# Performance work log

Measured on AMD Instinct MI355X. Metric: run time of the kernel, lower is better.

The kernel has to match this reference:

```python
import jax, jax.numpy as jnp
import numpy as np

EMBED_DIM = 768
Q_DIM = 64
V_DIM = 64
WINDOW_SIZE = 3


def setup_inputs() -> dict:
    key = jax.random.key(0)
    ks = jax.random.split(key, 7)
    B, N = 4, 4096
    s = 1.0 / np.sqrt(EMBED_DIM)
    x = jax.random.normal(ks[0], (B, N, EMBED_DIM), dtype=jnp.float32)
    Wq = jax.random.normal(ks[1], (EMBED_DIM, Q_DIM), dtype=jnp.float32) * s
    bq = jax.random.normal(ks[2], (Q_DIM,), dtype=jnp.float32) * 0.01
    Wk = jax.random.normal(ks[3], (EMBED_DIM, Q_DIM), dtype=jnp.float32) * s
    bk = jax.random.normal(ks[4], (Q_DIM,), dtype=jnp.float32) * 0.01
    Wv = jax.random.normal(ks[5], (EMBED_DIM, V_DIM), dtype=jnp.float32) * s
    bv = jax.random.normal(ks[6], (V_DIM,), dtype=jnp.float32) * 0.01
    return {"x": x, "Wq": Wq, "bq": bq, "Wk": Wk, "bk": bk, "Wv": Wv, "bv": bv}


def reference(x, Wq, bq, Wk, bk, Wv, bv):
    # Faithful translation of SliddingWindowAttention.forward, including the
    # original's quirk: diagonal scores are written into columns 0..window_size-1
    # of a full (B, N, N) zero matrix, softmax is taken over ALL N columns
    # (zeros included), and the result is matmul'd with V.
    B, N, _ = x.shape
    Q = x @ Wq + bq  # (B, N, Q_DIM)
    K = x @ Wk + bk  # (B, N, Q_DIM)
    V = x @ Wv + bv  # (B, N, V_DIM)

    half = WINDOW_SIZE // 2
    columns = jnp.zeros((B, N, N), dtype=x.dtype)
    for idx, di in enumerate(range(-half, half + 1)):
        # diagonal offset di: pair row i with column j = i + di (valid rows only)
        rows = np.arange(max(0, -di), N - max(0, di))
        cols_j = rows + di
        c = jnp.einsum('bid,bid->bi', Q[:, rows, :], K[:, cols_j, :])
        columns = columns.at[:, rows, idx].set(c)

    attn = jax.nn.softmax(columns, axis=2)  # (B, N, N)
    return attn @ V  # (B, N, V_DIM)
```

## Files before the change

### kernel.cpp

```cpp
#include <hip/hip_runtime.h>
#include <hip/hip_bf16.h>
#include <math.h>

#define EMBED 768
#define NTOK  4096
#define NB    4
#define ROWS  16384
#define CN    192

typedef __attribute__((ext_vector_type(8))) short bf16x8;
typedef __attribute__((ext_vector_type(8))) unsigned short u16x8;
typedef __attribute__((ext_vector_type(4))) float f32x4;

__device__ inline void split2(float f, short& h, short& l) {
  union { float f; unsigned u; } a; a.f = f;
  unsigned r = (a.u + 0x7FFFu + ((a.u >> 16) & 1u)) & 0xFFFF0000u;
  h = (short)(r >> 16);
  union { unsigned u; float f; } hf; hf.u = r;
  union { float f; unsigned u; } b; b.f = f - hf.f;
  l = (short)((b.u + 0x7FFFu + ((b.u >> 16) & 1u)) >> 16);
}

__global__ __launch_bounds__(256) void wprep(const float* __restrict__ Wq,
                                             const float* __restrict__ Wk,
                                             const float* __restrict__ Wv,
                                             unsigned short* __restrict__ Wt,
                                             float* __restrict__ Vsum) {
  __shared__ float tile[32 * 64];
  const int b   = blockIdx.x;
  const int mat = b / 24;
  const int ks  = b - mat * 24;
  const float* W = (mat == 0) ? Wq : (mat == 1) ? Wk : Wv;
  const int t = threadIdx.x;

  const float4* src = (const float4*)(W + ks * 2048);
  ((float4*)tile)[t]       = src[t];
  ((float4*)tile)[t + 256] = src[t + 256];
  __syncthreads();

  const int q    = t >> 6;
  const int nloc = t & 63;
  u16x8 hv, lv;
#pragma unroll
  for (int j = 0; j < 8; ++j) {
    short h, l;
    split2(tile[(q * 8 + j) * 64 + nloc], h, l);
    hv[j] = (unsigned short)h;
    lv[j] = (unsigned short)l;
  }
  const size_t base = (size_t)ks * 12288 + (size_t)q * 1536 + (size_t)(mat * 64 + nloc) * 8;
  *(u16x8*)(Wt + base)        = hv;
  *(u16x8*)(Wt + base + 6144) = lv;

  if (b == 0 && t < NB * 64) Vsum[t] = 0.f;
}


__device__ inline void splitHW(float f, short& h, short& l) {
  __hip_bfloat16 hb = __float2bfloat16(f);
  float hf = __bfloat162float(hb);
  __hip_bfloat16 lb = __float2bfloat16(f - hf);
  h = __builtin_bit_cast(short, hb);
  l = __builtin_bit_cast(short, lb);
}

__device__ inline void cvt8hw(const float4 f0, const float4 f1, bf16x8& h, bf16x8& l) {
  short hh, ll;
  splitHW(f0.x, hh, ll); h[0] = hh; l[0] = ll;
  splitHW(f0.y, hh, ll); h[1] = hh; l[1] = ll;
  splitHW(f0.z, hh, ll); h[2] = hh; l[2] = ll;
  splitHW(f0.w, hh, ll); h[3] = hh; l[3] = ll;
  splitHW(f1.x, hh, ll); h[4] = hh; l[4] = ll;
  splitHW(f1.y, hh, ll); h[5] = hh; l[5] = ll;
  splitHW(f1.z, hh, ll); h[6] = hh; l[6] = ll;
  splitHW(f1.w, hh, ll); h[7] = hh; l[7] = ll;
}

#define LOADB(H0, L0, H1, L1, H2, L2, KS) do {                        \
    const bf16x8* _p = (const bf16x8*)(Bb + (size_t)(KS) * 12288);    \
    H0 = _p[0];  L0 = _p[768];                                        \
    H1 = _p[16]; L1 = _p[784];                                        \
    H2 = _p[32]; L2 = _p[800];                                        \
  } while (0)

#define LOADA(A0, A1, KS) do {                                        \
    A0 = *(const float4*)(xa + (KS) * 32);                            \
    A1 = *(const float4*)(xa + (KS) * 32 + 4);                        \
  } while (0)

#define COMPUTE(A0, A1, H0, L0, H1, L1, H2, L2) do {                              \
    bf16x8 ah, al;                                                                \
    cvt8hw(A0, A1, ah, al);                                                       \
    acc0 = __builtin_amdgcn_mfma_f32_16x16x32_bf16(ah, H0, acc0, 0, 0, 0);        \
    acc1 = __builtin_amdgcn_mfma_f32_16x16x32_bf16(ah, H1, acc1, 0, 0, 0);        \
    acc2 = __builtin_amdgcn_mfma_f32_16x16x32_bf16(ah, H2, acc2, 0, 0, 0);        \
    acc0 = __builtin_amdgcn_mfma_f32_16x16x32_bf16(ah, L0, acc0, 0, 0, 0);        \
    acc1 = __builtin_amdgcn_mfma_f32_16x16x32_bf16(ah, L1, acc1, 0, 0, 0);        \
    acc2 = __builtin_amdgcn_mfma_f32_16x16x32_bf16(ah, L2, acc2, 0, 0, 0);        \
    acc0 = __builtin_amdgcn_mfma_f32_16x16x32_bf16(al, H0, acc0, 0, 0, 0);        \
    acc1 = __builtin_amdgcn_mfma_f32_16x16x32_bf16(al, H1, acc1, 0, 0, 0);        \
    acc2 = __builtin_amdgcn_mfma_f32_16x16x32_bf16(al, H2, acc2, 0, 0, 0);        \
  } while (0)

__global__ __launch_bounds__(512, 4) void qkv_mfma(const float* __restrict__ x,
                                                   const unsigned short* __restrict__ Wtu,
                                                   const float* __restrict__ bq,
                                                   const float* __restrict__ bk,
                                                   const float* __restrict__ bv,
                                                   float* __restrict__ C,
                                                   float* __restrict__ Vsum) {
  const int tid  = threadIdx.x;
  const int lane = tid & 63;
  const int wv   = tid >> 6;
  const int mh   = wv & 1;
  const int wn   = wv >> 1;
  const int ml   = lane & 15;
  const int q    = lane >> 4;
  const int r0   = blockIdx.x * 32;

  f32x4 acc0 = {0.f,0.f,0.f,0.f}, acc1 = {0.f,0.f,0.f,0.f}, acc2 = {0.f,0.f,0.f,0.f};

  const float* xa = x + (size_t)(r0 + mh * 16 + ml) * EMBED + q * 8;
  const unsigned short* Bb = Wtu + q * 1536 + (wn * 48 + ml) * 8;

  bf16x8 h0, l0, h1, l1, h2, l2;
  bf16x8 g0, m0, g1, m1, g2, m2;
  float4 a0, a1, b0, b1;

  LOADB(h0, l0, h1, l1, h2, l2, 0);
  LOADA(a0, a1, 0);

  for (int ks = 0; ks < 24; ks += 2) {
    LOADB(g0, m0, g1, m1, g2, m2, ks + 1);
    LOADA(b0, b1, ks + 1);
    COMPUTE(a0, a1, h0, l0, h1, l1, h2, l2);
    if (ks < 22) {
      LOADB(h0, l0, h1, l1, h2, l2, ks + 2);
      LOADA(a0, a1, ks + 2);
    }
    COMPUTE(b0, b1, g0, m0, g1, m1, g2, m2);
  }

#define EPI(NT, ACC) do {                                                   \
    const int n = wn * 48 + (NT) * 16 + ml;                                 \
    const float bias = (n < 64) ? bq[n] : (n < 128) ? bk[n - 64] : bv[n - 128]; \
    const int row = r0 + mh * 16 + q * 4;                                   \
    C[(size_t)(row + 0) * CN + n] = ACC[0] + bias;                          \
    C[(size_t)(row + 1) * CN + n] = ACC[1] + bias;                          \
    C[(size_t)(row + 2) * CN + n] = ACC[2] + bias;                          \
    C[(size_t)(row + 3) * CN + n] = ACC[3] + bias;                          \
  } while (0)

  EPI(0, acc0); EPI(1, acc1); EPI(2, acc2);

#define VS(NT, ACC) do {                                                    \
    const int n = wn * 48 + (NT) * 16 + ml;                                 \
    if (n >= 128) {                                                         \
      float s = ACC[0] + ACC[1] + ACC[2] + ACC[3] + 4.f * bv[n - 128];      \
      s += __shfl_xor(s, 16, 64);                                           \
      s += __shfl_xor(s, 32, 64);                                           \
      if (q == 0) atomicAdd(&Vsum[(r0 >> 12) * 64 + (n - 128)], s);         \
    }                                                                       \
  } while (0)

  VS(0, acc0); VS(1, acc1); VS(2, acc2);
}

__global__ __launch_bounds__(256) void attn_kernel(const float* __restrict__ C,
                                                   const float* __restrict__ Vsum,
                                                   float* __restrict__ out) {
  const int t    = threadIdx.x;
  const int lane = t & 63;
  const int wave = t >> 6;
  const int r = blockIdx.x * 4 + wave;
  const int b = r >> 12;
  const int i = r & (NTOK - 1);

  const float q  = C[(size_t)r * CN + lane];
  const float kc = C[(size_t)r * CN + 64 + lane];
  float km = 0.f, kp = 0.f;
  if (i > 0)        km = C[(size_t)(r - 1) * CN + 64 + lane];
  if (i < NTOK - 1) kp = C[(size_t)(r + 1) * CN + 64 + lane];

  float p0 = q * km, p1 = q * kc, p2 = q * kp;
#pragma unroll
  for (int off = 32; off > 0; off >>= 1) {
    p0 += __shfl_xor(p0, off, 64);
    p1 += __shfl_xor(p1, off, 64);
    p2 += __shfl_xor(p2, off, 64);
  }

  const float s0 = (i > 0) ? p0 : 0.f;
  const float s1 = p1;
  const float s2 = (i < NTOK - 1) ? p2 : 0.f;
  const float m  = fmaxf(fmaxf(s0, s1), fmaxf(s2, 0.f));
  const float e0 = expf(s0 - m);
  const float e1 = expf(s1 - m);
  const float e2 = expf(s2 - m);
  const float ez = expf(-m);
  const float Z  = e0 + e1 + e2 + (float)(NTOK - 3) * ez;

  const size_t vb = ((size_t)b * NTOK) * CN + 128;
  const float v0 = C[vb + lane];
  const float v1 = C[vb + CN + lane];
  const float v2 = C[vb + 2 * (size_t)CN + lane];
  const float vs = Vsum[b * 64 + lane];

  out[(size_t)r * 64 + lane] =
      (e0 * v0 + e1 * v1 + e2 * v2 + ez * (vs - v0 - v1 - v2)) / Z;
}

extern "C" void kernel_launch(void* const* d_in, const int* in_sizes, int n_in,
                              void* d_out, int out_size, void* d_ws, size_t ws_size,
                              hipStream_t stream) {
  const float* x  = (const float*)d_in[0];
  const float* Wq = (const float*)d_in[1];
  const float* bq = (const float*)d_in[2];
  const float* Wk = (const float*)d_in[3];
  const float* bk = (const float*)d_in[4];
  const float* Wv = (const float*)d_in[5];
  const float* bv = (const float*)d_in[6];
  float* out = (float*)d_out;

  float* C    = (float*)d_ws;
  float* Vsum = C + (size_t)ROWS * CN;
  unsigned short* Wt = (unsigned short*)(Vsum + NB * 64);

  wprep<<<72, 256, 0, stream>>>(Wq, Wk, Wv, Wt, Vsum);
  qkv_mfma<<<512, 512, 0, stream>>>(x, Wt, bq, bk, bv, C, Vsum);
  attn_kernel<<<ROWS / 4, 256, 0, stream>>>(C, Vsum, out);
}
```

Baseline: 140.6 us.

## Split K across wave pairs in QKV MFMA kernel with LDS reduction

Each block now handles 16 rows instead of 32. The two waves per N-slice split the 768-wide K dimension in half, and partial sums are reduced through shared memory before the epilogue. This doubles the grid to 1024 blocks, raises launch bounds to 6 blocks per SM, and drops the manual double-buffered prefetch in favour of a simple loop. The aim is more parallelism and occupancy to hide memory latency. In exchange each weight tile is reused by fewer rows, so weight loads per output row double, and the kernel adds a barrier and LDS traffic.

```diff
diff --git a/kernel.cpp b/kernel.cpp
--- a/kernel.cpp
+++ b/kernel.cpp
@@ -76,75 +76,73 @@
   splitHW(f1.w, hh, ll); h[7] = hh; l[7] = ll;
 }
 
-#define LOADB(H0, L0, H1, L1, H2, L2, KS) do {                        \
-    const bf16x8* _p = (const bf16x8*)(Bb + (size_t)(KS) * 12288);    \
-    H0 = _p[0];  L0 = _p[768];                                        \
-    H1 = _p[16]; L1 = _p[784];                                        \
-    H2 = _p[32]; L2 = _p[800];                                        \
-  } while (0)
-
-#define LOADA(A0, A1, KS) do {                                        \
-    A0 = *(const float4*)(xa + (KS) * 32);                            \
-    A1 = *(const float4*)(xa + (KS) * 32 + 4);                        \
-  } while (0)
-
-#define COMPUTE(A0, A1, H0, L0, H1, L1, H2, L2) do {                              \
-    bf16x8 ah, al;                                                                \
-    cvt8hw(A0, A1, ah, al);                                                       \
-    acc0 = __builtin_amdgcn_mfma_f32_16x16x32_bf16(ah, H0, acc0, 0, 0, 0);        \
-    acc1 = __builtin_amdgcn_mfma_f32_16x16x32_bf16(ah, H1, acc1, 0, 0, 0);        \
-    acc2 = __builtin_amdgcn_mfma_f32_16x16x32_bf16(ah, H2, acc2, 0, 0, 0);        \
-    acc0 = __builtin_amdgcn_mfma_f32_16x16x32_bf16(ah, L0, acc0, 0, 0, 0);        \
-    acc1 = __builtin_amdgcn_mfma_f32_16x16x32_bf16(ah, L1, acc1, 0, 0, 0);        \
-    acc2 = __builtin_amdgcn_mfma_f32_16x16x32_bf16(ah, L2, acc2, 0, 0, 0);        \
-    acc0 = __builtin_amdgcn_mfma_f32_16x16x32_bf16(al, H0, acc0, 0, 0, 0);        \
-    acc1 = __builtin_amdgcn_mfma_f32_16x16x32_bf16(al, H1, acc1, 0, 0, 0);        \
-    acc2 = __builtin_amdgcn_mfma_f32_16x16x32_bf16(al, H2, acc2, 0, 0, 0);        \
-  } while (0)
-
-__global__ __launch_bounds__(512, 4) void qkv_mfma(const float* __restrict__ x,
+__global__ __launch_bounds__(512, 6) void qkv_mfma(const float* __restrict__ x,
                                                    const unsigned short* __restrict__ Wtu,
                                                    const float* __restrict__ bq,
                                                    const float* __restrict__ bk,
                                                    const float* __restrict__ bv,
                                                    float* __restrict__ C,
                                                    float* __restrict__ Vsum) {
+  __shared__ float ms[4][16][48];
+
   const int tid  = threadIdx.x;
   const int lane = tid & 63;
   const int wv   = tid >> 6;
-  const int mh   = wv & 1;
   const int wn   = wv >> 1;
+  const int kh   = wv & 1;
   const int ml   = lane & 15;
   const int q    = lane >> 4;
-  const int r0   = blockIdx.x * 32;
+  const int r0   = blockIdx.x * 16;
 
   f32x4 acc0 = {0.f,0.f,0.f,0.f}, acc1 = {0.f,0.f,0.f,0.f}, acc2 = {0.f,0.f,0.f,0.f};
 
-  const float* xa = x + (size_t)(r0 + mh * 16 + ml) * EMBED + q * 8;
-  const unsigned short* Bb = Wtu + q * 1536 + (wn * 48 + ml) * 8;
-
-  bf16x8 h0, l0, h1, l1, h2, l2;
-  bf16x8 g0, m0, g1, m1, g2, m2;
-  float4 a0, a1, b0, b1;
-
-  LOADB(h0, l0, h1, l1, h2, l2, 0);
-  LOADA(a0, a1, 0);
-
-  for (int ks = 0; ks < 24; ks += 2) {
-    LOADB(g0, m0, g1, m1, g2, m2, ks + 1);
-    LOADA(b0, b1, ks + 1);
-    COMPUTE(a0, a1, h0, l0, h1, l1, h2, l2);
-    if (ks < 22) {
-      LOADB(h0, l0, h1, l1, h2, l2, ks + 2);
-      LOADA(a0, a1, ks + 2);
+  const float*          xa = x   + (size_t)(r0 + ml) * EMBED + kh * 384 + q * 8;
+  const unsigned short* Bb = Wtu + (size_t)(kh * 12) * 12288 + q * 1536 + (wn * 48 + ml) * 8;
+
+  for (int ks = 0; ks < 12; ++ks) {
+    const bf16x8* bp = (const bf16x8*)Bb;
+    bf16x8 bh0 = bp[0],  bl0 = bp[768];
+    bf16x8 bh1 = bp[16], bl1 = bp[784];
+    bf16x8 bh2 = bp[32], bl2 = bp[800];
+    float4 a0 = *(const float4*)xa;
+    float4 a1 = *(const float4*)(xa + 4);
+    bf16x8 ah, al;
+    cvt8hw(a0, a1, ah, al);
+    acc0 = __builtin_amdgcn_mfma_f32_16x16x32_bf16(ah, bh0, acc0, 0, 0, 0);
+    acc1 = __builtin_amdgcn_mfma_f32_16x16x32_bf16(ah, bh1, acc1, 0, 0, 0);
+    acc2 = __builtin_amdgcn_mfma_f32_16x16x32_bf16(ah, bh2, acc2, 0, 0, 0);
+    acc0 = __builtin_amdgcn_mfma_f32_16x16x32_bf16(ah, bl0, acc0, 0, 0, 0);
+    acc1 = __builtin_amdgcn_mfma_f32_16x16x32_bf16(ah, bl1, acc1, 0, 0, 0);
+    acc2 = __builtin_amdgcn_mfma_f32_16x16x32_bf16(ah, bl2, acc2, 0, 0, 0);
+    acc0 = __builtin_amdgcn_mfma_f32_16x16x32_bf16(al, bh0, acc0, 0, 0, 0);
+    acc1 = __builtin_amdgcn_mfma_f32_16x16x32_bf16(al, bh1, acc1, 0, 0, 0);
+    acc2 = __builtin_amdgcn_mfma_f32_16x16x32_bf16(al, bh2, acc2, 0, 0, 0);
+    xa += 32;
+    Bb += 12288;
+  }
+
+  if (kh == 1) {
+#pragma unroll
+    for (int reg = 0; reg < 4; ++reg) {
+      ms[wn][q * 4 + reg][0 * 16 + ml] = acc0[reg];
+      ms[wn][q * 4 + reg][1 * 16 + ml] = acc1[reg];
+      ms[wn][q * 4 + reg][2 * 16 + ml] = acc2[reg];
     }
-    COMPUTE(b0, b1, g0, m0, g1, m1, g2, m2);
+  }
+  __syncthreads();
+  if (kh == 1) return;
+
+#pragma unroll
+  for (int reg = 0; reg < 4; ++reg) {
+    acc0[reg] += ms[wn][q * 4 + reg][0 * 16 + ml];
+    acc1[reg] += ms[wn][q * 4 + reg][1 * 16 + ml];
+    acc2[reg] += ms[wn][q * 4 + reg][2 * 16 + ml];
   }
 
 #define EPI(NT, ACC) do {                                                   \
     const int n = wn * 48 + (NT) * 16 + ml;                                 \
     const float bias = (n < 64) ? bq[n] : (n < 128) ? bk[n - 64] : bv[n - 128]; \
-    const int row = r0 + mh * 16 + q * 4;                                   \
+    const int row = r0 + q * 4;                                             \
     C[(size_t)(row + 0) * CN + n] = ACC[0] + bias;                          \
     C[(size_t)(row + 1) * CN + n] = ACC[1] + bias;                          \
     C[(size_t)(row + 2) * CN + n] = ACC[2] + bias;                          \
@@ -227,6 +225,6 @@
   unsigned short* Wt = (unsigned short*)(Vsum + NB * 64);
 
   wprep<<<72, 256, 0, stream>>>(Wq, Wk, Wv, Wt, Vsum);
-  qkv_mfma<<<512, 512, 0, stream>>>(x, Wt, bq, bk, bv, C, Vsum);
+  qkv_mfma<<<ROWS / 16, 512, 0, stream>>>(x, Wt, bq, bk, bv, C, Vsum);
   attn_kernel<<<ROWS / 4, 256, 0, stream>>>(C, Vsum, out);
 }
```

New measurement: 141.3 us. Within noise of the previous version (+0.5%).
